# Kernel optimization log

Hardware: AMD Instinct MI355X
Metric: run time of the kernel (lower is better)

Reference implementation:

```python
import jax, jax.numpy as jnp
import numpy as np

NUM_EMBEDDINGS = 1024  # num_gestures
EMBEDDING_DIM = 512    # win_size * num_pellets = 32 * 16


def setup_inputs() -> dict:
    key = jax.random.key(0)
    k1, k2 = jax.random.split(key)
    inputs = jax.random.normal(k1, (64, 512, EMBEDDING_DIM), dtype=jnp.float32)
    weight = jax.random.normal(k2, (NUM_EMBEDDINGS, EMBEDDING_DIM), dtype=jnp.float32)
    return {"inputs": inputs, "weight": weight}


def reference(inputs, weight):
    input_shape = inputs.shape
    flat = inputs.reshape(-1, EMBEDDING_DIM)  # [N, D]
    distances = (
        jnp.sum(flat * flat, axis=1, keepdims=True)
        + jnp.sum(weight * weight, axis=1)
        - 2.0 * (flat @ weight.T)
    )
    encoding_indices = jnp.argmin(distances, axis=1)  # [N]
    # one-hot @ weight is just a gather of codebook rows
    quantized = weight[encoding_indices].reshape(input_shape)
    loss_vq = jnp.mean((quantized - inputs) ** 2)
    return loss_vq
```

## Files before the change

kernel.cpp:

```cpp
#include <hip/hip_runtime.h>
#include <hip/hip_bf16.h>
#include <stdint.h>

typedef __attribute__((ext_vector_type(4))) int i32x4;

#define N_ROWS  32768
#define N_CODES 1024
#define DIM     512
#define BK      64
#define NT      (DIM / BK)

typedef const __attribute__((address_space(1))) uint32_t guint;
typedef __attribute__((address_space(3))) uint32_t luint;
static __device__ __forceinline__ void gl_lds16(const char* g, char* l) {
    __builtin_amdgcn_global_load_lds((guint*)g, (luint*)l, 16, 0, 0);
}

static __device__ __forceinline__ int q8(float v) {
    int q = __float2int_rn(v * 32.0f);
    return max(-127, min(127, q));
}

__global__ void __launch_bounds__(256)
convertXW(const float* __restrict__ X, const float* __restrict__ W,
          char* __restrict__ Xq, char* __restrict__ Wq,
          float* __restrict__ xnorm, float* __restrict__ wnorm) {
    const int lane = threadIdx.x & 63;
    const int sub  = threadIdx.x >> 6;
    const float* src; char* dst; float* nrm; int row;
    if (blockIdx.x < 8192) {
        row = blockIdx.x * 4 + sub;
        src = X; dst = Xq; nrm = xnorm;
    } else {
        row = (blockIdx.x - 8192) * 4 + sub;
        src = W; dst = Wq; nrm = wnorm;
    }
    const float4* p = (const float4*)(src + (size_t)row * DIM + lane * 8);
    float4 a = p[0], b = p[1];
    uint32_t lo = (uint32_t)(q8(a.x) & 0xFF)
                | ((uint32_t)(q8(a.y) & 0xFF) << 8)
                | ((uint32_t)(q8(a.z) & 0xFF) << 16)
                | ((uint32_t)(q8(a.w) & 0xFF) << 24);
    uint32_t hi = (uint32_t)(q8(b.x) & 0xFF)
                | ((uint32_t)(q8(b.y) & 0xFF) << 8)
                | ((uint32_t)(q8(b.z) & 0xFF) << 16)
                | ((uint32_t)(q8(b.w) & 0xFF) << 24);
    *(uint2*)(dst + (size_t)row * DIM + lane * 8) = make_uint2(lo, hi);
    float s = a.x*a.x + a.y*a.y + a.z*a.z + a.w*a.w
            + b.x*b.x + b.y*b.y + b.z*b.z + b.w*b.w;
    #pragma unroll
    for (int d = 1; d < 64; d <<= 1) s += __shfl_xor(s, d);
    if (lane == 0) nrm[row] = s;
}

__global__ void __launch_bounds__(256, 4)
gemm_argmin(const char* __restrict__ Xq, const char* __restrict__ Wq,
            const float* __restrict__ wnorm, uint32_t* __restrict__ keys) {
    __shared__ __align__(16) char As[2][128 * BK];
    __shared__ __align__(16) char Bs[2][128 * BK];

    const int tid  = threadIdx.x;
    const int lane = tid & 63;
    const int wave = tid >> 6;
    const int wr = wave >> 1, wc = wave & 1;
    const int lr = lane & 15, kg = lane >> 4;

    const int bid = blockIdx.x;
    const int colBase = ((bid >> 3) & 7) * 128;
    const int rowBase = ((bid & 7) * 32 + (bid >> 6)) * 128;

    const int ssw = ((tid & 3) ^ ((tid >> 3) & 3)) * 16;
    const char* aS = Xq + (size_t)(rowBase + (tid >> 2)) * DIM + ssw;
    const char* bS = Wq + (size_t)(colBase + (tid >> 2)) * DIM + ssw;

#define STAGE(buf, t) do {                                                    \
    gl_lds16(aS + (t) * BK,           &As[buf][tid * 16]);                    \
    gl_lds16(aS + 64*DIM + (t) * BK,  &As[buf][tid * 16 + 4096]);             \
    gl_lds16(bS + (t) * BK,           &Bs[buf][tid * 16]);                    \
    gl_lds16(bS + 64*DIM + (t) * BK,  &Bs[buf][tid * 16 + 4096]);             \
  } while (0)

    i32x4 acc[4][4];
    #pragma unroll
    for (int m = 0; m < 4; ++m)
        #pragma unroll
        for (int n = 0; n < 4; ++n) acc[m][n] = (i32x4)0;

    const int fq = (kg ^ ((lr >> 1) & 3)) * 16;

    STAGE(0, 0);
    __syncthreads();

    #pragma unroll
    for (int t = 0; t < NT; ++t) {
        const int cur = t & 1;
        if (t < NT - 1) STAGE(cur ^ 1, t + 1);
        i32x4 aF[4], bF[4];
        #pragma unroll
        for (int m = 0; m < 4; ++m)
            aF[m] = *(const i32x4*)&As[cur][(wr*64 + m*16 + lr) * BK + fq];
        #pragma unroll
        for (int n = 0; n < 4; ++n)
            bF[n] = *(const i32x4*)&Bs[cur][(wc*64 + n*16 + lr) * BK + fq];
        #pragma unroll
        for (int m = 0; m < 4; ++m)
            #pragma unroll
            for (int n = 0; n < 4; ++n)
                acc[m][n] = __builtin_amdgcn_mfma_i32_16x16x64_i8(
                    aF[m], bF[n], acc[m][n], 0, 0, 0);
        __syncthreads();
    }
#undef STAGE

    float wn[4]; int wcol[4];
    #pragma unroll
    for (int n = 0; n < 4; ++n) {
        wcol[n] = colBase + wc*64 + n*16 + lr;
        wn[n] = wnorm[wcol[n]];
    }
    const int chunk = (colBase >> 6) + wc;
    #pragma unroll
    for (int m = 0; m < 4; ++m) {
        #pragma unroll
        for (int r = 0; r < 4; ++r) {
            uint32_t best = 0xFFFFFFFFu;
            #pragma unroll
            for (int n = 0; n < 4; ++n) {
                float sc = wn[n] - (float)acc[m][n][r] * 0.001953125f;
                uint32_t u = __float_as_uint(sc);
                u = (u & 0x80000000u) ? ~u : (u | 0x80000000u);
                uint32_t key = (u & ~1023u) | (uint32_t)wcol[n];
                best = min(best, key);
            }
            #pragma unroll
            for (int d = 1; d < 16; d <<= 1)
                best = min(best, (uint32_t)__shfl_xor((int)best, d));
            if (lr == 0) {
                const int row = rowBase + wr*64 + m*16 + kg*4 + r;
                keys[(size_t)row * 16 + chunk] = best;
            }
        }
    }
}

__global__ void __launch_bounds__(256)
reduce_loss(const uint32_t* __restrict__ keys, const float* __restrict__ xnorm,
            float* __restrict__ partial) {
    __shared__ float sm[256];
    const int row = blockIdx.x * 256 + threadIdx.x;
    const uint4* kp = (const uint4*)(keys + (size_t)row * 16);
    uint4 k0 = kp[0], k1 = kp[1], k2 = kp[2], k3 = kp[3];
    uint32_t mk = min(min(min(k0.x, k0.y), min(k0.z, k0.w)),
                      min(min(k1.x, k1.y), min(k1.z, k1.w)));
    mk = min(mk, min(min(min(k2.x, k2.y), min(k2.z, k2.w)),
                     min(min(k3.x, k3.y), min(k3.z, k3.w))));
    uint32_t sb = mk & ~1023u;
    float sc = (sb & 0x80000000u) ? __uint_as_float(sb ^ 0x80000000u)
                                  : __uint_as_float(~sb);
    sm[threadIdx.x] = xnorm[row] + sc;
    __syncthreads();
    for (int st = 128; st > 0; st >>= 1) {
        if (threadIdx.x < st) sm[threadIdx.x] += sm[threadIdx.x + st];
        __syncthreads();
    }
    if (threadIdx.x == 0) partial[blockIdx.x] = sm[0];
}

__global__ void __launch_bounds__(128)
finalize(const float* __restrict__ partial, float* __restrict__ out) {
    __shared__ double sm[128];
    sm[threadIdx.x] = (double)partial[threadIdx.x];
    __syncthreads();
    for (int st = 64; st > 0; st >>= 1) {
        if (threadIdx.x < st) sm[threadIdx.x] += sm[threadIdx.x + st];
        __syncthreads();
    }
    if (threadIdx.x == 0)
        out[0] = (float)(sm[0] / (double)((size_t)N_ROWS * DIM));
}

extern "C" void kernel_launch(void* const* d_in, const int* in_sizes, int n_in,
                              void* d_out, int out_size, void* d_ws, size_t ws_size,
                              hipStream_t stream) {
    const float* X = (const float*)d_in[0];
    const float* W = (const float*)d_in[1];
    char* ws = (char*)d_ws;
    char*     Xq      = ws;
    char*     Wq      = ws + 16777216;
    float*    wnorm   = (float*)(ws + 17301504);
    float*    xnorm   = (float*)(ws + 17305600);
    uint32_t* keys    = (uint32_t*)(ws + 17436672);
    float*    partial = (float*)(ws + 19533824);
    float*    out     = (float*)d_out;

    convertXW<<<8192 + N_CODES / 4, 256, 0, stream>>>(X, W, Xq, Wq, xnorm, wnorm);
    gemm_argmin<<<2048, 256, 0, stream>>>(Xq, Wq, wnorm, keys);
    reduce_loss<<<N_ROWS / 256, 256, 0, stream>>>(keys, xnorm, partial);
    finalize<<<1, 128, 0, stream>>>(partial, out);
}
```

Before: 53.50 us.

## Fuse argmin and loss reduction into GEMM with per-block row tile over all codes

Result: faster. 50.41 us (-5.8%).

```diff
diff --git a/kernel.cpp b/kernel.cpp
--- a/kernel.cpp
+++ b/kernel.cpp
@@ -7,8 +7,6 @@
 #define N_ROWS  32768
 #define N_CODES 1024
 #define DIM     512
-#define BK      64
-#define NT      (DIM / BK)
 
 typedef const __attribute__((address_space(1))) uint32_t guint;
 typedef __attribute__((address_space(3))) uint32_t luint;
@@ -53,125 +51,128 @@
     if (lane == 0) nrm[row] = s;
 }
 
-__global__ void __launch_bounds__(256, 4)
+__global__ void __launch_bounds__(256, 2)
 gemm_argmin(const char* __restrict__ Xq, const char* __restrict__ Wq,
-            const float* __restrict__ wnorm, uint32_t* __restrict__ keys) {
-    __shared__ __align__(16) char As[2][128 * BK];
-    __shared__ __align__(16) char Bs[2][128 * BK];
+            const float* __restrict__ wnorm, const float* __restrict__ xnorm,
+            float* __restrict__ partial) {
+    __shared__ __align__(16) char As[8 * 4096];
+    __shared__ __align__(16) char Bs[4 * 3 * 2048];
 
     const int tid  = threadIdx.x;
     const int lane = tid & 63;
     const int wave = tid >> 6;
-    const int wr = wave >> 1, wc = wave & 1;
     const int lr = lane & 15, kg = lane >> 4;
 
     const int bid = blockIdx.x;
-    const int colBase = ((bid >> 3) & 7) * 128;
-    const int rowBase = ((bid & 7) * 32 + (bid >> 6)) * 128;
+    const int rowBase = ((bid & 7) * 64 + (bid >> 3)) * 64;
+    const int colW = wave * 256;
 
-    const int ssw = ((tid & 3) ^ ((tid >> 3) & 3)) * 16;
-    const char* aS = Xq + (size_t)(rowBase + (tid >> 2)) * DIM + ssw;
-    const char* bS = Wq + (size_t)(colBase + (tid >> 2)) * DIM + ssw;
+    const int ssw = ((lane & 3) ^ ((lane >> 3) & 3)) * 16;
+    const char* aS = Xq + (size_t)(rowBase + wave * 16 + (lane >> 2)) * DIM + ssw;
+    const char* bS = Wq + (size_t)(colW + (lane >> 2)) * DIM + ssw;
+    char* bD = Bs + wave * 6144 + lane * 16;
 
-#define STAGE(buf, t) do {                                                    \
-    gl_lds16(aS + (t) * BK,           &As[buf][tid * 16]);                    \
-    gl_lds16(aS + 64*DIM + (t) * BK,  &As[buf][tid * 16 + 4096]);             \
-    gl_lds16(bS + (t) * BK,           &Bs[buf][tid * 16]);                    \
-    gl_lds16(bS + 64*DIM + (t) * BK,  &Bs[buf][tid * 16 + 4096]);             \
+#define STAGE_B(s) do {                                                       \
+    const int ct_ = (s) >> 3, kt_ = (s) & 7, buf_ = (s) % 3;                  \
+    gl_lds16(bS + (size_t)(ct_ * 32) * DIM + kt_ * 64,      bD + buf_ * 2048);\
+    gl_lds16(bS + (size_t)(ct_ * 32 + 16) * DIM + kt_ * 64, bD + buf_ * 2048 + 1024); \
   } while (0)
 
-    i32x4 acc[4][4];
+    #pragma unroll
+    for (int kt = 0; kt < 8; ++kt)
+        gl_lds16(aS + kt * 64, As + kt * 4096 + wave * 1024 + lane * 16);
+    STAGE_B(0);
+    STAGE_B(1);
+    asm volatile("s_waitcnt vmcnt(2)" ::: "memory");
+    __syncthreads();
+
+    i32x4 acc[4][2];
+    #pragma unroll
+    for (int m = 0; m < 4; ++m) { acc[m][0] = (i32x4)0; acc[m][1] = (i32x4)0; }
+    uint32_t runKey[4][4];
     #pragma unroll
     for (int m = 0; m < 4; ++m)
         #pragma unroll
-        for (int n = 0; n < 4; ++n) acc[m][n] = (i32x4)0;
+        for (int r = 0; r < 4; ++r) runKey[m][r] = 0xFFFFFFFFu;
 
     const int fq = (kg ^ ((lr >> 1) & 3)) * 16;
+    const char* bR = Bs + wave * 6144;
 
-    STAGE(0, 0);
-    __syncthreads();
-
-    #pragma unroll
-    for (int t = 0; t < NT; ++t) {
-        const int cur = t & 1;
-        if (t < NT - 1) STAGE(cur ^ 1, t + 1);
-        i32x4 aF[4], bF[4];
+    for (int s = 0; s < 64; ++s) {
+        const int kt = s & 7, buf = s % 3;
+        i32x4 aF[4], bF[2];
         #pragma unroll
         for (int m = 0; m < 4; ++m)
-            aF[m] = *(const i32x4*)&As[cur][(wr*64 + m*16 + lr) * BK + fq];
+            aF[m] = *(const i32x4*)&As[kt * 4096 + (m * 16 + lr) * 64 + fq];
         #pragma unroll
-        for (int n = 0; n < 4; ++n)
-            bF[n] = *(const i32x4*)&Bs[cur][(wc*64 + n*16 + lr) * BK + fq];
+        for (int n = 0; n < 2; ++n)
+            bF[n] = *(const i32x4*)&bR[buf * 2048 + (n * 16 + lr) * 64 + fq];
+        if (s + 2 < 64) STAGE_B(s + 2);
         #pragma unroll
         for (int m = 0; m < 4; ++m)
             #pragma unroll
-            for (int n = 0; n < 4; ++n)
+            for (int n = 0; n < 2; ++n)
                 acc[m][n] = __builtin_amdgcn_mfma_i32_16x16x64_i8(
                     aF[m], bF[n], acc[m][n], 0, 0, 0);
-        __syncthreads();
+        if (kt == 7) {
+            const int ct = s >> 3;
+            #pragma unroll
+            for (int n = 0; n < 2; ++n) {
+                const int wcol = colW + ct * 32 + n * 16 + lr;
+                const float wn = wnorm[wcol];
+                #pragma unroll
+                for (int m = 0; m < 4; ++m)
+                    #pragma unroll
+                    for (int r = 0; r < 4; ++r) {
+                        float sc = wn - (float)acc[m][n][r] * 0.001953125f;
+                        uint32_t u = __float_as_uint(sc);
+                        u = (u & 0x80000000u) ? ~u : (u | 0x80000000u);
+                        runKey[m][r] = min(runKey[m][r],
+                                           (u & ~1023u) | (uint32_t)wcol);
+                    }
+            }
+            #pragma unroll
+            for (int m = 0; m < 4; ++m) { acc[m][0] = (i32x4)0; acc[m][1] = (i32x4)0; }
+        }
+        if (s + 2 < 64)       asm volatile("s_waitcnt vmcnt(2)" ::: "memory");
+        else if (s == 62)     asm volatile("s_waitcnt vmcnt(0)" ::: "memory");
     }
-#undef STAGE
+#undef STAGE_B
 
-    float wn[4]; int wcol[4];
+    uint32_t* kbuf = (uint32_t*)(Bs + wave * 6144);
     #pragma unroll
-    for (int n = 0; n < 4; ++n) {
-        wcol[n] = colBase + wc*64 + n*16 + lr;
-        wn[n] = wnorm[wcol[n]];
-    }
-    const int chunk = (colBase >> 6) + wc;
-    #pragma unroll
-    for (int m = 0; m < 4; ++m) {
+    for (int m = 0; m < 4; ++m)
         #pragma unroll
         for (int r = 0; r < 4; ++r) {
-            uint32_t best = 0xFFFFFFFFu;
-            #pragma unroll
-            for (int n = 0; n < 4; ++n) {
-                float sc = wn[n] - (float)acc[m][n][r] * 0.001953125f;
-                uint32_t u = __float_as_uint(sc);
-                u = (u & 0x80000000u) ? ~u : (u | 0x80000000u);
-                uint32_t key = (u & ~1023u) | (uint32_t)wcol[n];
-                best = min(best, key);
-            }
+            uint32_t k = runKey[m][r];
             #pragma unroll
             for (int d = 1; d < 16; d <<= 1)
-                best = min(best, (uint32_t)__shfl_xor((int)best, d));
-            if (lr == 0) {
-                const int row = rowBase + wr*64 + m*16 + kg*4 + r;
-                keys[(size_t)row * 16 + chunk] = best;
-            }
+                k = min(k, (uint32_t)__shfl_xor((int)k, d));
+            if (lr == 0) kbuf[m * 16 + kg * 4 + r] = k;
         }
+    __syncthreads();
+
+    if (wave == 0) {
+        const uint32_t* k0 = (const uint32_t*)(Bs);
+        uint32_t k = min(min(k0[lane], k0[1536 + lane]),
+                         min(k0[3072 + lane], k0[4608 + lane]));
+        uint32_t sb = k & ~1023u;
+        float sc = (sb & 0x80000000u) ? __uint_as_float(sb ^ 0x80000000u)
+                                      : __uint_as_float(~sb);
+        float v = xnorm[rowBase + lane] + sc;
+        #pragma unroll
+        for (int d = 1; d < 64; d <<= 1) v += __shfl_xor(v, d);
+        if (lane == 0) partial[bid] = v;
     }
 }
 
 __global__ void __launch_bounds__(256)
-reduce_loss(const uint32_t* __restrict__ keys, const float* __restrict__ xnorm,
-            float* __restrict__ partial) {
-    __shared__ float sm[256];
-    const int row = blockIdx.x * 256 + threadIdx.x;
-    const uint4* kp = (const uint4*)(keys + (size_t)row * 16);
-    uint4 k0 = kp[0], k1 = kp[1], k2 = kp[2], k3 = kp[3];
-    uint32_t mk = min(min(min(k0.x, k0.y), min(k0.z, k0.w)),
-                      min(min(k1.x, k1.y), min(k1.z, k1.w)));
-    mk = min(mk, min(min(min(k2.x, k2.y), min(k2.z, k2.w)),
-                     min(min(k3.x, k3.y), min(k3.z, k3.w))));
-    uint32_t sb = mk & ~1023u;
-    float sc = (sb & 0x80000000u) ? __uint_as_float(sb ^ 0x80000000u)
-                                  : __uint_as_float(~sb);
-    sm[threadIdx.x] = xnorm[row] + sc;
+finalize(const float* __restrict__ partial, float* __restrict__ out) {
+    __shared__ double sm[256];
+    sm[threadIdx.x] = (double)partial[threadIdx.x]
+                    + (double)partial[threadIdx.x + 256];
     __syncthreads();
     for (int st = 128; st > 0; st >>= 1) {
-        if (threadIdx.x < st) sm[threadIdx.x] += sm[threadIdx.x + st];
-        __syncthreads();
-    }
-    if (threadIdx.x == 0) partial[blockIdx.x] = sm[0];
-}
-
-__global__ void __launch_bounds__(128)
-finalize(const float* __restrict__ partial, float* __restrict__ out) {
-    __shared__ double sm[128];
-    sm[threadIdx.x] = (double)partial[threadIdx.x];
-    __syncthreads();
-    for (int st = 64; st > 0; st >>= 1) {
         if (threadIdx.x < st) sm[threadIdx.x] += sm[threadIdx.x + st];
         __syncthreads();
     }
@@ -185,16 +186,14 @@
     const float* X = (const float*)d_in[0];
     const float* W = (const float*)d_in[1];
     char* ws = (char*)d_ws;
-    char*     Xq      = ws;
-    char*     Wq      = ws + 16777216;
-    float*    wnorm   = (float*)(ws + 17301504);
-    float*    xnorm   = (float*)(ws + 17305600);
-    uint32_t* keys    = (uint32_t*)(ws + 17436672);
-    float*    partial = (float*)(ws + 19533824);
-    float*    out     = (float*)d_out;
+    char*   Xq      = ws;
+    char*   Wq      = ws + 16777216;
+    float*  wnorm   = (float*)(ws + 17301504);
+    float*  xnorm   = (float*)(ws + 17305600);
+    float*  partial = (float*)(ws + 17436672);
+    float*  out     = (float*)d_out;
 
     convertXW<<<8192 + N_CODES / 4, 256, 0, stream>>>(X, W, Xq, Wq, xnorm, wnorm);
-    gemm_argmin<<<2048, 256, 0, stream>>>(Xq, Wq, wnorm, keys);
-    reduce_loss<<<N_ROWS / 256, 256, 0, stream>>>(keys, xnorm, partial);
-    finalize<<<1, 128, 0, stream>>>(partial, out);
+    gemm_argmin<<<512, 256, 0, stream>>>(Xq, Wq, wnorm, xnorm, partial);
+    finalize<<<1, 256, 0, stream>>>(partial, out);
 }
```
